# Performance work log

Measured on AMD Instinct MI355X. Metric: run time of the kernel, lower is better.

## Reference

```python
import math
import jax, jax.numpy as jnp
import numpy as np

B, C, L = 4, 768, 8192      # batch, num_channels(width), seq_len
E, O = 33, 64               # emb_dim, order (filter MLP width)


def setup_inputs() -> dict:
    key = jax.random.key(0)
    ks = jax.random.split(key, 8)
    x = jax.random.normal(ks[0], (B, C, L), jnp.float32)
    bias = jax.random.normal(ks[1], (C,), jnp.float32)

    # PositionalEmbedding: z param (constant init) and time_emb t
    t = jnp.linspace(0.0, 1.0, L, dtype=jnp.float32)[None, :, None]   # [1,L,1]
    bands = (E - 1) // 2
    t_r = jnp.linspace(0.0, L - 1.0, L)[None, :, None]
    w = 2.0 * math.pi * t_r / L
    f = jnp.linspace(1e-4, bands - 1.0, bands)[None, None]
    zc = jnp.exp(-1j * f * w)
    z = jnp.concatenate([t, zc.real, zc.imag], axis=2).astype(jnp.float32)  # [1,L,E]

    # ExponentialModulation deltas param (deterministic init)
    target, fast_pct, slow_pct = 0.01, 0.3, 1.5
    max_decay = math.log(target) / fast_pct
    min_decay = math.log(target) / slow_pct
    deltas = jnp.linspace(min_decay, max_decay, C, dtype=jnp.float32)[None, None]  # [1,1,C]

    sc = 0.02
    w0 = jax.random.normal(ks[2], (E, O), jnp.float32) * sc
    b0 = jnp.zeros((O,), jnp.float32)
    w1 = jax.random.normal(ks[3], (O, O), jnp.float32) * sc
    b1 = jnp.zeros((O,), jnp.float32)
    w2 = jax.random.normal(ks[4], (O, O), jnp.float32) * sc
    b2 = jnp.zeros((O,), jnp.float32)
    wout = jax.random.normal(ks[5], (O, C), jnp.float32) * sc  # final Dense, no bias
    freq = jnp.ones((1, O), jnp.float32)  # Sin freq param, shared across all Sin uses
    return dict(x=x, bias=bias, z=z, t=t, deltas=deltas, freq=freq,
                w0=w0, b0=b0, w1=w1, b1=b1, w2=w2, b2=b2, wout=wout)


def reference(x, bias, z, t, deltas, freq, w0, b0, w1, b1, w2, b2, wout):
    seq_len = x.shape[-1]
    # implicit filter MLP: [Dense -> Sin] x3 -> Dense(no bias)
    h = jnp.sin(freq * (z @ w0 + b0))
    h = jnp.sin(freq * (h @ w1 + b1))
    h = jnp.sin(freq * (h @ w2 + b2))
    h = h @ wout                                   # [1, L, C]
    # exponential modulation (shift = 0)
    h = h * jnp.exp(-t * jnp.abs(deltas))          # [1, L, C]
    k = h[0].T                                     # [C, L]
    # FFT long convolution
    fft_size = 2 * seq_len
    k_f = jnp.fft.rfft(k, n=fft_size) / fft_size   # [C, L+1] complex
    u_f = jnp.fft.rfft(x, n=fft_size)              # [B, C, L+1] complex
    y = jnp.fft.irfft(u_f * k_f, n=fft_size, norm='forward')[..., :seq_len]
    out = y + x * bias[:, None]
    return out.astype(x.dtype)
```

## Files before the change

### kernel.cpp

```cpp
#include <hip/hip_runtime.h>
#include <math.h>

#define L_SEQ 8192
#define NFFT  16384
#define N2    8192
#define N4    4096
#define CCH   768
#define BB    4
#define EDIM  33
#define ODIM  64
#define BLK   512

#define C_PI8 0.9238795325112867f
#define S_PI8 0.3826834323650898f
#define C_PI4 0.7071067811865476f

#define ALPHA 1.52587890625e-05f

constexpr int rev4_12c(int v) {
  int r = 0;
  for (int i = 0; i < 6; ++i) { r = (r << 2) | (v & 3); v >>= 2; }
  return r;
}
constexpr int pos8c(int f) { return ((f & 1) << 12) | rev4_12c(f >> 1); }
constexpr int swzc(int i) { return i ^ ((i >> 4) & 15) ^ ((i >> 8) & 15); }

__device__ __forceinline__ float2 cadd(float2 a, float2 b) { return make_float2(a.x + b.x, a.y + b.y); }
__device__ __forceinline__ float2 csub(float2 a, float2 b) { return make_float2(a.x - b.x, a.y - b.y); }
__device__ __forceinline__ float2 cmul(float2 a, float2 b) {
  return make_float2(fmaf(a.x, b.x, -a.y * b.y), fmaf(a.x, b.y, a.y * b.x));
}
__device__ __forceinline__ float2 cmulc(float2 a, float2 w) {
  return make_float2(fmaf(a.x, w.x, a.y * w.y), fmaf(a.y, w.x, -a.x * w.y));
}
__device__ __forceinline__ float2 cconj(float2 a) { return make_float2(a.x, -a.y); }

__device__ __forceinline__ void dif4(float2& x0, float2& x1, float2& x2, float2& x3,
                                     float2 w1, float2 w2, float2 w3) {
  float2 a = cadd(x0, x2), b = csub(x0, x2);
  float2 c = cadd(x1, x3), d = csub(x1, x3);
  x0 = cadd(a, c);
  x1 = cmul(make_float2(b.x + d.y, b.y - d.x), w1);
  x2 = cmul(csub(a, c), w2);
  x3 = cmul(make_float2(b.x - d.y, b.y + d.x), w3);
}
__device__ __forceinline__ void dif4_nw(float2& x0, float2& x1, float2& x2, float2& x3) {
  float2 a = cadd(x0, x2), b = csub(x0, x2);
  float2 c = cadd(x1, x3), d = csub(x1, x3);
  x0 = cadd(a, c);
  x1 = make_float2(b.x + d.y, b.y - d.x);
  x2 = csub(a, c);
  x3 = make_float2(b.x - d.y, b.y + d.x);
}
__device__ __forceinline__ void dit4(float2& x0, float2& x1, float2& x2, float2& x3,
                                     float2 w1, float2 w2, float2 w3) {
  float2 t0 = x0, t1 = cmulc(x1, w1), t2 = cmulc(x2, w2), t3 = cmulc(x3, w3);
  float2 a = cadd(t0, t2), b = csub(t0, t2);
  float2 c = cadd(t1, t3), d = csub(t1, t3);
  x0 = cadd(a, c);
  x1 = make_float2(b.x - d.y, b.y + d.x);
  x2 = csub(a, c);
  x3 = make_float2(b.x + d.y, b.y - d.x);
}
__device__ __forceinline__ void dit4_nw(float2& x0, float2& x1, float2& x2, float2& x3) {
  float2 a = cadd(x0, x2), b = csub(x0, x2);
  float2 c = cadd(x1, x3), d = csub(x1, x3);
  x0 = cadd(a, c);
  x1 = make_float2(b.x - d.y, b.y + d.x);
  x2 = csub(a, c);
  x3 = make_float2(b.x + d.y, b.y - d.x);
}

__device__ __forceinline__ void ld3(const float4* __restrict__ tab, int idx,
                                    float2& w1, float2& w2, float2& w3) {
  float4 a = tab[2 * idx];
  float4 b = tab[2 * idx + 1];
  w1 = make_float2(a.x, a.y);
  w2 = make_float2(a.z, a.w);
  w3 = make_float2(b.x, b.y);
}

__global__ void twiddle_kernel(float2* __restrict__ tw, float4* __restrict__ T4,
                               float4* __restrict__ T16, float4* __restrict__ T64,
                               float4* __restrict__ T256) {
  const int r = blockIdx.x * blockDim.x + threadIdx.x;
  const float C = (float)(6.283185307179586476925286766559 / 16384.0);
  if (r < NFFT) {
    float s, c;
    sincosf(C * (float)r, &s, &c);
    tw[r] = make_float2(c, -s);
  }
  const int j = r - NFFT;
  float4* tab = nullptr;
  int idx = 0, e = 0;
  if (j >= 0 && j < 1024)      { tab = T4;   idx = j;        e = 4 * (j & 255) + 1024 * (j >> 8); }
  else if (j >= 1024 && j < 1280) { tab = T16;  idx = j - 1024; e = 16 * idx; }
  else if (j >= 1280 && j < 1344) { tab = T64;  idx = j - 1280; e = 64 * (idx & 15) + 1024 * (idx >> 4); }
  else if (j >= 1344 && j < 1360) { tab = T256; idx = j - 1344; e = 256 * idx; }
  if (tab) {
    float s1, c1, s2, c2, s3, c3;
    sincosf(C * (float)e, &s1, &c1);
    sincosf(C * (float)(2 * e), &s2, &c2);
    sincosf(C * (float)(3 * e), &s3, &c3);
    tab[2 * idx]     = make_float4(c1, -s1, c2, -s2);
    tab[2 * idx + 1] = make_float4(c3, -s3, 0.f, 0.f);
  }
}

#define ML 16
__global__ __launch_bounds__(128) void mlp_kernel(
    const float* __restrict__ z, const float* __restrict__ freq,
    const float* __restrict__ w0, const float* __restrict__ b0,
    const float* __restrict__ w1, const float* __restrict__ b1,
    const float* __restrict__ w2, const float* __restrict__ b2,
    float* __restrict__ h)
{
  __shared__ float zs[ML][EDIM];
  __shared__ float hsA[ML][ODIM + 1];
  __shared__ float hsB[ML][ODIM + 1];
  const int tid = threadIdx.x;
  const int l0 = blockIdx.x * ML;
  const int lrow = tid & 15;
  const int oc = (tid >> 4) * 8;

  for (int idx = tid; idx < ML * EDIM; idx += 128) {
    int r = idx / EDIM, cc = idx - r * EDIM;
    zs[r][cc] = z[(l0 + r) * EDIM + cc];
  }
  __syncthreads();

  float acc[8], fr[8];
#pragma unroll
  for (int k = 0; k < 8; ++k) { fr[k] = freq[oc + k]; acc[k] = b0[oc + k]; }
#pragma unroll 4
  for (int e = 0; e < EDIM; ++e) {
    const float zv = zs[lrow][e];
#pragma unroll
    for (int j = 0; j < 2; ++j) {
      float4 w4 = *(const float4*)&w0[e * ODIM + oc + 4 * j];
      acc[4*j+0] = fmaf(zv, w4.x, acc[4*j+0]);
      acc[4*j+1] = fmaf(zv, w4.y, acc[4*j+1]);
      acc[4*j+2] = fmaf(zv, w4.z, acc[4*j+2]);
      acc[4*j+3] = fmaf(zv, w4.w, acc[4*j+3]);
    }
  }
#pragma unroll
  for (int k = 0; k < 8; ++k) hsA[lrow][oc + k] = sinf(fr[k] * acc[k]);
  __syncthreads();

#pragma unroll
  for (int k = 0; k < 8; ++k) acc[k] = b1[oc + k];
#pragma unroll 4
  for (int i = 0; i < ODIM; ++i) {
    const float hv = hsA[lrow][i];
#pragma unroll
    for (int j = 0; j < 2; ++j) {
      float4 w4 = *(const float4*)&w1[i * ODIM + oc + 4 * j];
      acc[4*j+0] = fmaf(hv, w4.x, acc[4*j+0]);
      acc[4*j+1] = fmaf(hv, w4.y, acc[4*j+1]);
      acc[4*j+2] = fmaf(hv, w4.z, acc[4*j+2]);
      acc[4*j+3] = fmaf(hv, w4.w, acc[4*j+3]);
    }
  }
#pragma unroll
  for (int k = 0; k < 8; ++k) hsB[lrow][oc + k] = sinf(fr[k] * acc[k]);
  __syncthreads();

#pragma unroll
  for (int k = 0; k < 8; ++k) acc[k] = b2[oc + k];
#pragma unroll 4
  for (int i = 0; i < ODIM; ++i) {
    const float hv = hsB[lrow][i];
#pragma unroll
    for (int j = 0; j < 2; ++j) {
      float4 w4 = *(const float4*)&w2[i * ODIM + oc + 4 * j];
      acc[4*j+0] = fmaf(hv, w4.x, acc[4*j+0]);
      acc[4*j+1] = fmaf(hv, w4.y, acc[4*j+1]);
      acc[4*j+2] = fmaf(hv, w4.z, acc[4*j+2]);
      acc[4*j+3] = fmaf(hv, w4.w, acc[4*j+3]);
    }
  }
#pragma unroll
  for (int k = 0; k < 8; ++k)
    h[(size_t)(oc + k) * L_SEQ + l0 + lrow] = sinf(fr[k] * acc[k]);
}

__global__ __launch_bounds__(256) void kout_kernel(
    const float* __restrict__ h, const float* __restrict__ wout,
    const float* __restrict__ t, const float* __restrict__ deltas,
    float* __restrict__ k)
{
  __shared__ float hT[ODIM][64];
  __shared__ float wT[ODIM][64];
  const int lb = blockIdx.x % (L_SEQ / 64);
  const int cb = blockIdx.x / (L_SEQ / 64);
  const int l0 = lb * 64, c0 = cb * 64;
  const int tid = threadIdx.x;
  for (int i = tid; i < ODIM * 16; i += 256) {
    int o = i >> 4, lq = (i & 15) * 4;
    *(float4*)&hT[o][lq] = *(const float4*)&h[(size_t)o * L_SEQ + l0 + lq];
  }
  for (int i = tid; i < ODIM * 16; i += 256) {
    int o = i >> 4, cq = (i & 15) * 4;
    *(float4*)&wT[o][cq] = *(const float4*)&wout[(size_t)o * CCH + c0 + cq];
  }
  __syncthreads();
  const int li = tid & 15, ci = tid >> 4;
  float acc[4][4];
#pragma unroll
  for (int a = 0; a < 4; ++a)
#pragma unroll
    for (int b = 0; b < 4; ++b) acc[a][b] = 0.f;
#pragma unroll 8
  for (int o = 0; o < ODIM; ++o) {
    float4 h4 = *(const float4*)&hT[o][li * 4];
    float4 w4 = *(const float4*)&wT[o][ci * 4];
    const float ha[4] = {h4.x, h4.y, h4.z, h4.w};
    const float wa[4] = {w4.x, w4.y, w4.z, w4.w};
#pragma unroll
    for (int a = 0; a < 4; ++a)
#pragma unroll
      for (int b = 0; b < 4; ++b) acc[a][b] = fmaf(ha[a], wa[b], acc[a][b]);
  }
  float4 t4 = *(const float4*)&t[l0 + li * 4];
  const float ta[4] = {t4.x, t4.y, t4.z, t4.w};
#pragma unroll
  for (int b = 0; b < 4; ++b) {
    const int c = c0 + ci * 4 + b;
    const float dl = fabsf(deltas[c]);
    float4 r;
    r.x = acc[0][b] * expf(-ta[0] * dl);
    r.y = acc[1][b] * expf(-ta[1] * dl);
    r.z = acc[2][b] * expf(-ta[2] * dl);
    r.w = acc[3][b] * expf(-ta[3] * dl);
    *(float4*)&k[(size_t)c * L_SEQ + l0 + li * 4] = r;
  }
}

__device__ __forceinline__ void load_row(float2 xr[4][4], const float2* __restrict__ src,
                                         const float2* __restrict__ tw, int tid) {
  const int h = tid >> 8, u = tid & 255;
#pragma unroll
  for (int s = 0; s < 4; ++s)
#pragma unroll
    for (int t = 0; t < 4; ++t) xr[s][t] = src[u + s * 1024 + t * 256];
  if (h) {
#pragma unroll
    for (int s = 0; s < 4; ++s)
#pragma unroll
      for (int t = 0; t < 4; ++t) xr[s][t] = cmul(xr[s][t], tw[2 * (u + s * 1024 + t * 256)]);
  }
}

__device__ __forceinline__ void fwd_roundA(float2* Z, float2 xr[4][4],
                                           const float4* __restrict__ T4,
                                           const float4* __restrict__ T16, int tid) {
  const int h = tid >> 8, u = tid & 255;
#pragma unroll
  for (int t = 0; t < 4; ++t) {
    float2 w1, w2, w3;
    ld3(T4, t * 256 + u, w1, w2, w3);
    dif4(xr[0][t], xr[1][t], xr[2][t], xr[3][t], w1, w2, w3);
  }
  {
    float2 w1, w2, w3;
    ld3(T16, u, w1, w2, w3);
#pragma unroll
    for (int s = 0; s < 4; ++s) dif4(xr[s][0], xr[s][1], xr[s][2], xr[s][3], w1, w2, w3);
  }
  const int sb = swzc((h << 12) + u);
#pragma unroll
  for (int s = 0; s < 4; ++s)
#pragma unroll
    for (int t = 0; t < 4; ++t) Z[sb ^ swzc(s * 1024 + t * 256)] = xr[s][t];
}

__device__ __forceinline__ void fwd_roundB(float2* Z, const float4* __restrict__ T64,
                                           const float4* __restrict__ T256, int tid) {
  const int u = tid & 15, g = (tid >> 4) & 15, h = tid >> 8;
  const int sb = swzc((h << 12) + (g << 8) + u);
  float2 e[4][4];
#pragma unroll
  for (int s = 0; s < 4; ++s)
#pragma unroll
    for (int t = 0; t < 4; ++t) e[s][t] = Z[sb ^ swzc(s * 64 + t * 16)];
#pragma unroll
  for (int t = 0; t < 4; ++t) {
    float2 w1, w2, w3;
    ld3(T64, t * 16 + u, w1, w2, w3);
    dif4(e[0][t], e[1][t], e[2][t], e[3][t], w1, w2, w3);
  }
  {
    float2 w1, w2, w3;
    ld3(T256, u, w1, w2, w3);
#pragma unroll
    for (int s = 0; s < 4; ++s) dif4(e[s][0], e[s][1], e[s][2], e[s][3], w1, w2, w3);
  }
#pragma unroll
  for (int s = 0; s < 4; ++s)
#pragma unroll
    for (int t = 0; t < 4; ++t) Z[sb ^ swzc(s * 64 + t * 16)] = e[s][t];
}

__device__ __forceinline__ void fwd_roundC(float2* Z, int tid) {
  const int h = tid >> 8, jp = tid & 255;
  const int sb = swzc((h << 12) + (jp << 4));
  float2 e[4][4];
#pragma unroll
  for (int s = 0; s < 4; ++s)
#pragma unroll
    for (int t = 0; t < 4; ++t) e[s][t] = Z[sb ^ (s * 4 + t)];
  dif4_nw(e[0][0], e[1][0], e[2][0], e[3][0]);
  dif4(e[0][1], e[1][1], e[2][1], e[3][1],
       make_float2(C_PI8, -S_PI8), make_float2(C_PI4, -C_PI4), make_float2(S_PI8, -C_PI8));
  dif4(e[0][2], e[1][2], e[2][2], e[3][2],
       make_float2(C_PI4, -C_PI4), make_float2(0.f, -1.f), make_float2(-C_PI4, -C_PI4));
  dif4(e[0][3], e[1][3], e[2][3], e[3][3],
       make_float2(S_PI8, -C_PI8), make_float2(-C_PI4, -C_PI4), make_float2(-C_PI8, S_PI8));
#pragma unroll
  for (int s = 0; s < 4; ++s) dif4_nw(e[s][0], e[s][1], e[s][2], e[s][3]);
#pragma unroll
  for (int s = 0; s < 4; ++s)
#pragma unroll
    for (int t = 0; t < 4; ++t) Z[sb ^ (s * 4 + t)] = e[s][t];
}

__device__ __forceinline__ void inv_roundA(float2* Z, int tid) {
  const int h = tid >> 8, jp = tid & 255;
  const int sb = swzc((h << 12) + (jp << 4));
  float2 e[4][4];
#pragma unroll
  for (int s = 0; s < 4; ++s)
#pragma unroll
    for (int t = 0; t < 4; ++t) e[s][t] = Z[sb ^ (s * 4 + t)];
#pragma unroll
  for (int s = 0; s < 4; ++s) dit4_nw(e[s][0], e[s][1], e[s][2], e[s][3]);
  dit4_nw(e[0][0], e[1][0], e[2][0], e[3][0]);
  dit4(e[0][1], e[1][1], e[2][1], e[3][1],
       make_float2(C_PI8, -S_PI8), make_float2(C_PI4, -C_PI4), make_float2(S_PI8, -C_PI8));
  dit4(e[0][2], e[1][2], e[2][2], e[3][2],
       make_float2(C_PI4, -C_PI4), make_float2(0.f, -1.f), make_float2(-C_PI4, -C_PI4));
  dit4(e[0][3], e[1][3], e[2][3], e[3][3],
       make_float2(S_PI8, -C_PI8), make_float2(-C_PI4, -C_PI4), make_float2(-C_PI8, S_PI8));
#pragma unroll
  for (int s = 0; s < 4; ++s)
#pragma unroll
    for (int t = 0; t < 4; ++t) Z[sb ^ (s * 4 + t)] = e[s][t];
}

__device__ __forceinline__ void inv_roundB(float2* Z, const float4* __restrict__ T64,
                                           const float4* __restrict__ T256, int tid) {
  const int u = tid & 15, g = (tid >> 4) & 15, h = tid >> 8;
  const int sb = swzc((h << 12) + (g << 8) + u);
  float2 e[4][4];
#pragma unroll
  for (int s = 0; s < 4; ++s)
#pragma unroll
    for (int t = 0; t < 4; ++t) e[s][t] = Z[sb ^ swzc(s * 64 + t * 16)];
  {
    float2 w1, w2, w3;
    ld3(T256, u, w1, w2, w3);
#pragma unroll
    for (int s = 0; s < 4; ++s) dit4(e[s][0], e[s][1], e[s][2], e[s][3], w1, w2, w3);
  }
#pragma unroll
  for (int t = 0; t < 4; ++t) {
    float2 w1, w2, w3;
    ld3(T64, t * 16 + u, w1, w2, w3);
    dit4(e[0][t], e[1][t], e[2][t], e[3][t], w1, w2, w3);
  }
#pragma unroll
  for (int s = 0; s < 4; ++s)
#pragma unroll
    for (int t = 0; t < 4; ++t) Z[sb ^ swzc(s * 64 + t * 16)] = e[s][t];
}

__device__ __forceinline__ void inv_roundC(float2* Z, const float4* __restrict__ T4,
                                           const float4* __restrict__ T16, int tid) {
  const int h = tid >> 8, u = tid & 255;
  const int sb = swzc((h << 12) + u);
  float2 e[4][4];
#pragma unroll
  for (int s = 0; s < 4; ++s)
#pragma unroll
    for (int t = 0; t < 4; ++t) e[s][t] = Z[sb ^ swzc(s * 1024 + t * 256)];
  {
    float2 w1, w2, w3;
    ld3(T16, u, w1, w2, w3);
#pragma unroll
    for (int s = 0; s < 4; ++s) dit4(e[s][0], e[s][1], e[s][2], e[s][3], w1, w2, w3);
  }
#pragma unroll
  for (int t = 0; t < 4; ++t) {
    float2 w1, w2, w3;
    ld3(T4, t * 256 + u, w1, w2, w3);
    dit4(e[0][t], e[1][t], e[2][t], e[3][t], w1, w2, w3);
  }
#pragma unroll
  for (int s = 0; s < 4; ++s)
#pragma unroll
    for (int t = 0; t < 4; ++t) Z[sb ^ swzc(s * 1024 + t * 256)] = e[s][t];
}

__global__ __launch_bounds__(BLK, 4) void kfft_kernel(
    const float* __restrict__ kf, const float2* __restrict__ tw,
    const float4* __restrict__ T4, const float4* __restrict__ T16,
    const float4* __restrict__ T64, const float4* __restrict__ T256,
    float2* __restrict__ Kf)
{
  extern __shared__ float2 Z[];
  const int c = blockIdx.x, tid = threadIdx.x;
  const float2* k2 = (const float2*)(kf + (size_t)c * L_SEQ);
  float2 xr[4][4];
  load_row(xr, k2, tw, tid);
  fwd_roundA(Z, xr, T4, T16, tid);
  __syncthreads();
  fwd_roundB(Z, T64, T256, tid);
  __syncthreads();
  fwd_roundC(Z, tid);
  __syncthreads();

  float2* Kc = Kf + (size_t)c * N2;
  const int P0 = swzc(pos8c(tid));
  const int Q0 = swzc(pos8c(512 - tid));
  const float beta = 0.5f * ALPHA;
#pragma unroll
  for (int s2 = 0; s2 < 8; ++s2) {
    if (s2 == 0 && tid == 0) {
      float2 z0 = Z[0];
      Kc[0] = make_float2(ALPHA * (z0.x + z0.y), ALPHA * (z0.x - z0.y));
      float2 z4 = Z[2];
      Kc[N4] = make_float2(ALPHA * z4.x, -ALPHA * z4.y);
    } else {
      const int f = tid + s2 * BLK;
      const int p = P0 ^ swzc(pos8c(s2 * 512));
      const int pq = (tid == 0) ? swzc(pos8c(((16 - s2) * 512) & (N2 - 1)))
                                : (Q0 ^ swzc(pos8c((15 - s2) * 512)));
      float2 zf = Z[p], zg = Z[pq];
      float2 E = make_float2(beta * (zf.x + zg.x), beta * (zf.y - zg.y));
      float2 O = make_float2(beta * (zf.y + zg.y), beta * (zg.x - zf.x));
      float2 wO = cmul(tw[f], O);
      Kc[f]      = cadd(E, wO);
      Kc[N2 - f] = cconj(csub(E, wO));
    }
  }
}

__global__ __launch_bounds__(BLK, 4) void conv_kernel(
    const float* __restrict__ x, const float2* __restrict__ Kf,
    const float* __restrict__ bias, const float2* __restrict__ tw,
    const float4* __restrict__ T4, const float4* __restrict__ T16,
    const float4* __restrict__ T64, const float4* __restrict__ T256,
    float* __restrict__ out)
{
  extern __shared__ float2 Z[];
  const int tid = threadIdx.x;
  const int c = blockIdx.x % CCH;
  const int b = blockIdx.x / CCH;
  const float2* x2 = (const float2*)(x + (size_t)(b * CCH + c) * L_SEQ);
  const float2* Kc = Kf + (size_t)c * N2;

  float2 xr[4][4];
  load_row(xr, x2, tw, tid);
  fwd_roundA(Z, xr, T4, T16, tid);
  __syncthreads();
  fwd_roundB(Z, T64, T256, tid);
  __syncthreads();
  fwd_roundC(Z, tid);
  __syncthreads();

  const int P0 = swzc(pos8c(tid));
  const int Q0 = swzc(pos8c(512 - tid));
#pragma unroll
  for (int s2 = 0; s2 < 8; ++s2) {
    if (s2 == 0 && tid == 0) {
      float2 z0 = Z[0];
      float2 k0 = Kc[0];
      float2 k4 = Kc[N4];
      float Y0 = (z0.x + z0.y) * k0.x;
      float Y8 = (z0.x - z0.y) * k0.y;
      Z[0] = make_float2(2.f * (Y0 + Y8), 2.f * (Y0 - Y8));
      float2 z4 = Z[2];
      float2 Y4 = cmul(make_float2(z4.x, -z4.y), k4);
      Z[2] = make_float2(4.f * Y4.x, -4.f * Y4.y);
    } else {
      const int f = tid + s2 * BLK;
      const int fc = (N2 - f) & (N2 - 1);
      const int p = P0 ^ swzc(pos8c(s2 * 512));
      const int pq = (tid == 0) ? swzc(pos8c(((16 - s2) * 512) & (N2 - 1)))
                                : (Q0 ^ swzc(pos8c((15 - s2) * 512)));
      float2 k0 = Kc[f];
      float2 k1 = Kc[fc];
      float2 zf = Z[p], zg = Z[pq];
      float2 E = make_float2(zf.x + zg.x, zf.y - zg.y);
      float2 O = make_float2(zf.y + zg.y, zg.x - zf.x);
      float2 w = tw[f];
      float2 wO = cmul(w, O);
      float2 P = cadd(E, wO);
      float2 M = csub(E, wO);
      float2 Yf  = cmul(P, k0);
      float2 Ygc = cmul(M, cconj(k1));
      float2 A  = make_float2(Yf.x + Ygc.x, Yf.y + Ygc.y);
      float2 Bc = make_float2(Yf.x - Ygc.x, Yf.y - Ygc.y);
      float2 cb = cmulc(Bc, w);
      Z[p]  = make_float2(A.x - cb.y, A.y + cb.x);
      Z[pq] = make_float2(A.x + cb.y, -A.y + cb.x);
    }
  }
  __syncthreads();
  inv_roundA(Z, tid);
  __syncthreads();
  inv_roundB(Z, T64, T256, tid);
  __syncthreads();
  inv_roundC(Z, T4, T16, tid);
  __syncthreads();

  const float bc = bias[c];
  float2* o2 = (float2*)(out + (size_t)(b * CCH + c) * L_SEQ);
  const int E0 = swzc(tid);
#pragma unroll
  for (int j = 0; j < 8; ++j) {
    const int i = tid + j * 512;
    const int zi = E0 ^ swzc(j * 512);
    float2 a = Z[zi];
    float2 bb = cmulc(Z[zi ^ 4096], tw[2 * i]);
    float2 xv = x2[i];
    o2[i] = make_float2(a.x + bb.x + xv.x * bc, a.y + bb.y + xv.y * bc);
  }
}

extern "C" void kernel_launch(void* const* d_in, const int* in_sizes, int n_in,
                              void* d_out, int out_size, void* d_ws, size_t ws_size,
                              hipStream_t stream) {
  const float* x      = (const float*)d_in[0];
  const float* bias   = (const float*)d_in[1];
  const float* z      = (const float*)d_in[2];
  const float* t      = (const float*)d_in[3];
  const float* deltas = (const float*)d_in[4];
  const float* freq   = (const float*)d_in[5];
  const float* w0     = (const float*)d_in[6];
  const float* b0     = (const float*)d_in[7];
  const float* w1     = (const float*)d_in[8];
  const float* b1     = (const float*)d_in[9];
  const float* w2     = (const float*)d_in[10];
  const float* b2     = (const float*)d_in[11];
  const float* wout   = (const float*)d_in[12];
  float* out = (float*)d_out;

  char* p = (char*)d_ws;
  float2* tw   = (float2*)p;             p += (size_t)NFFT * sizeof(float2);
  float4* T4   = (float4*)p;             p += (size_t)1024 * 2 * sizeof(float4);
  float4* T16  = (float4*)p;             p += (size_t)256 * 2 * sizeof(float4);
  float4* T64  = (float4*)p;             p += (size_t)64 * 2 * sizeof(float4);
  float4* T256 = (float4*)p;             p += (size_t)16 * 2 * sizeof(float4);
  float*  h    = (float*)p;              p += (size_t)ODIM * L_SEQ * sizeof(float);
  float*  kfilt= (float*)p;              p += (size_t)CCH * L_SEQ * sizeof(float);
  float2* Kf   = (float2*)p;

  twiddle_kernel<<<70, 256, 0, stream>>>(tw, T4, T16, T64, T256);
  mlp_kernel<<<L_SEQ / ML, 128, 0, stream>>>(z, freq, w0, b0, w1, b1, w2, b2, h);
  kout_kernel<<<(L_SEQ / 64) * (CCH / 64), 256, 0, stream>>>(h, wout, t, deltas, kfilt);

  const size_t lds = (size_t)N2 * sizeof(float2);
  hipFuncSetAttribute(reinterpret_cast<const void*>(kfft_kernel),
                      hipFuncAttributeMaxDynamicSharedMemorySize, lds);
  hipFuncSetAttribute(reinterpret_cast<const void*>(conv_kernel),
                      hipFuncAttributeMaxDynamicSharedMemorySize, lds);
  kfft_kernel<<<CCH, BLK, lds, stream>>>(kfilt, tw, T4, T16, T64, T256, Kf);
  conv_kernel<<<BB * CCH, BLK, lds, stream>>>(x, Kf, bias, tw, T4, T16, T64, T256, out);
}
```

Before: 207.3 us.

## Restructure FFT into per-stage radix-4 passes with 1024-thread blocks

Replaces the register-heavy radix-16 rounds, where each thread holds a 4x4 tile, with six radix-4 stages done one at a time in LDS by 1024 threads, each thread processing two butterflies per stage. The first forward stage and the last inverse stage are fused with the global load and the store. The aim is fewer registers per thread and more resident threads to hide memory latency. The cost is twice as many barriers and LDS round trips, plus a 1024-thread block holding 64KB of LDS, which may limit occupancy.

```diff
diff --git a/kernel.cpp b/kernel.cpp
--- a/kernel.cpp
+++ b/kernel.cpp
@@ -9,11 +9,7 @@
 #define BB    4
 #define EDIM  33
 #define ODIM  64
-#define BLK   512
-
-#define C_PI8 0.9238795325112867f
-#define S_PI8 0.3826834323650898f
-#define C_PI4 0.7071067811865476f
+#define BLK2  1024
 
 #define ALPHA 1.52587890625e-05f
 
@@ -237,172 +233,120 @@
   }
 }
 
-__device__ __forceinline__ void load_row(float2 xr[4][4], const float2* __restrict__ src,
-                                         const float2* __restrict__ tw, int tid) {
-  const int h = tid >> 8, u = tid & 255;
-#pragma unroll
-  for (int s = 0; s < 4; ++s)
-#pragma unroll
-    for (int t = 0; t < 4; ++t) xr[s][t] = src[u + s * 1024 + t * 256];
-  if (h) {
-#pragma unroll
-    for (int s = 0; s < 4; ++s)
-#pragma unroll
-      for (int t = 0; t < 4; ++t) xr[s][t] = cmul(xr[s][t], tw[2 * (u + s * 1024 + t * 256)]);
-  }
-}
-
-__device__ __forceinline__ void fwd_roundA(float2* Z, float2 xr[4][4],
-                                           const float4* __restrict__ T4,
-                                           const float4* __restrict__ T16, int tid) {
-  const int h = tid >> 8, u = tid & 255;
-#pragma unroll
-  for (int t = 0; t < 4; ++t) {
-    float2 w1, w2, w3;
-    ld3(T4, t * 256 + u, w1, w2, w3);
-    dif4(xr[0][t], xr[1][t], xr[2][t], xr[3][t], w1, w2, w3);
-  }
-  {
-    float2 w1, w2, w3;
-    ld3(T16, u, w1, w2, w3);
-#pragma unroll
-    for (int s = 0; s < 4; ++s) dif4(xr[s][0], xr[s][1], xr[s][2], xr[s][3], w1, w2, w3);
-  }
-  const int sb = swzc((h << 12) + u);
-#pragma unroll
-  for (int s = 0; s < 4; ++s)
-#pragma unroll
-    for (int t = 0; t < 4; ++t) Z[sb ^ swzc(s * 1024 + t * 256)] = xr[s][t];
-}
-
-__device__ __forceinline__ void fwd_roundB(float2* Z, const float4* __restrict__ T64,
-                                           const float4* __restrict__ T256, int tid) {
-  const int u = tid & 15, g = (tid >> 4) & 15, h = tid >> 8;
-  const int sb = swzc((h << 12) + (g << 8) + u);
-  float2 e[4][4];
-#pragma unroll
-  for (int s = 0; s < 4; ++s)
-#pragma unroll
-    for (int t = 0; t < 4; ++t) e[s][t] = Z[sb ^ swzc(s * 64 + t * 16)];
-#pragma unroll
-  for (int t = 0; t < 4; ++t) {
-    float2 w1, w2, w3;
-    ld3(T64, t * 16 + u, w1, w2, w3);
-    dif4(e[0][t], e[1][t], e[2][t], e[3][t], w1, w2, w3);
-  }
-  {
-    float2 w1, w2, w3;
-    ld3(T256, u, w1, w2, w3);
-#pragma unroll
-    for (int s = 0; s < 4; ++s) dif4(e[s][0], e[s][1], e[s][2], e[s][3], w1, w2, w3);
-  }
-#pragma unroll
-  for (int s = 0; s < 4; ++s)
-#pragma unroll
-    for (int t = 0; t < 4; ++t) Z[sb ^ swzc(s * 64 + t * 16)] = e[s][t];
-}
-
-__device__ __forceinline__ void fwd_roundC(float2* Z, int tid) {
-  const int h = tid >> 8, jp = tid & 255;
-  const int sb = swzc((h << 12) + (jp << 4));
-  float2 e[4][4];
-#pragma unroll
-  for (int s = 0; s < 4; ++s)
-#pragma unroll
-    for (int t = 0; t < 4; ++t) e[s][t] = Z[sb ^ (s * 4 + t)];
-  dif4_nw(e[0][0], e[1][0], e[2][0], e[3][0]);
-  dif4(e[0][1], e[1][1], e[2][1], e[3][1],
-       make_float2(C_PI8, -S_PI8), make_float2(C_PI4, -C_PI4), make_float2(S_PI8, -C_PI8));
-  dif4(e[0][2], e[1][2], e[2][2], e[3][2],
-       make_float2(C_PI4, -C_PI4), make_float2(0.f, -1.f), make_float2(-C_PI4, -C_PI4));
-  dif4(e[0][3], e[1][3], e[2][3], e[3][3],
-       make_float2(S_PI8, -C_PI8), make_float2(-C_PI4, -C_PI4), make_float2(-C_PI8, S_PI8));
-#pragma unroll
-  for (int s = 0; s < 4; ++s) dif4_nw(e[s][0], e[s][1], e[s][2], e[s][3]);
-#pragma unroll
-  for (int s = 0; s < 4; ++s)
-#pragma unroll
-    for (int t = 0; t < 4; ++t) Z[sb ^ (s * 4 + t)] = e[s][t];
-}
-
-__device__ __forceinline__ void inv_roundA(float2* Z, int tid) {
-  const int h = tid >> 8, jp = tid & 255;
-  const int sb = swzc((h << 12) + (jp << 4));
-  float2 e[4][4];
-#pragma unroll
-  for (int s = 0; s < 4; ++s)
-#pragma unroll
-    for (int t = 0; t < 4; ++t) e[s][t] = Z[sb ^ (s * 4 + t)];
-#pragma unroll
-  for (int s = 0; s < 4; ++s) dit4_nw(e[s][0], e[s][1], e[s][2], e[s][3]);
-  dit4_nw(e[0][0], e[1][0], e[2][0], e[3][0]);
-  dit4(e[0][1], e[1][1], e[2][1], e[3][1],
-       make_float2(C_PI8, -S_PI8), make_float2(C_PI4, -C_PI4), make_float2(S_PI8, -C_PI8));
-  dit4(e[0][2], e[1][2], e[2][2], e[3][2],
-       make_float2(C_PI4, -C_PI4), make_float2(0.f, -1.f), make_float2(-C_PI4, -C_PI4));
-  dit4(e[0][3], e[1][3], e[2][3], e[3][3],
-       make_float2(S_PI8, -C_PI8), make_float2(-C_PI4, -C_PI4), make_float2(-C_PI8, S_PI8));
-#pragma unroll
-  for (int s = 0; s < 4; ++s)
-#pragma unroll
-    for (int t = 0; t < 4; ++t) Z[sb ^ (s * 4 + t)] = e[s][t];
-}
-
-__device__ __forceinline__ void inv_roundB(float2* Z, const float4* __restrict__ T64,
-                                           const float4* __restrict__ T256, int tid) {
-  const int u = tid & 15, g = (tid >> 4) & 15, h = tid >> 8;
-  const int sb = swzc((h << 12) + (g << 8) + u);
-  float2 e[4][4];
-#pragma unroll
-  for (int s = 0; s < 4; ++s)
-#pragma unroll
-    for (int t = 0; t < 4; ++t) e[s][t] = Z[sb ^ swzc(s * 64 + t * 16)];
-  {
-    float2 w1, w2, w3;
-    ld3(T256, u, w1, w2, w3);
-#pragma unroll
-    for (int s = 0; s < 4; ++s) dit4(e[s][0], e[s][1], e[s][2], e[s][3], w1, w2, w3);
-  }
-#pragma unroll
-  for (int t = 0; t < 4; ++t) {
-    float2 w1, w2, w3;
-    ld3(T64, t * 16 + u, w1, w2, w3);
-    dit4(e[0][t], e[1][t], e[2][t], e[3][t], w1, w2, w3);
-  }
-#pragma unroll
-  for (int s = 0; s < 4; ++s)
-#pragma unroll
-    for (int t = 0; t < 4; ++t) Z[sb ^ swzc(s * 64 + t * 16)] = e[s][t];
-}
-
-__device__ __forceinline__ void inv_roundC(float2* Z, const float4* __restrict__ T4,
-                                           const float4* __restrict__ T16, int tid) {
-  const int h = tid >> 8, u = tid & 255;
-  const int sb = swzc((h << 12) + u);
-  float2 e[4][4];
-#pragma unroll
-  for (int s = 0; s < 4; ++s)
-#pragma unroll
-    for (int t = 0; t < 4; ++t) e[s][t] = Z[sb ^ swzc(s * 1024 + t * 256)];
-  {
-    float2 w1, w2, w3;
-    ld3(T16, u, w1, w2, w3);
-#pragma unroll
-    for (int s = 0; s < 4; ++s) dit4(e[s][0], e[s][1], e[s][2], e[s][3], w1, w2, w3);
-  }
-#pragma unroll
-  for (int t = 0; t < 4; ++t) {
-    float2 w1, w2, w3;
-    ld3(T4, t * 256 + u, w1, w2, w3);
-    dit4(e[0][t], e[1][t], e[2][t], e[3][t], w1, w2, w3);
-  }
-#pragma unroll
-  for (int s = 0; s < 4; ++s)
-#pragma unroll
-    for (int t = 0; t < 4; ++t) Z[sb ^ swzc(s * 1024 + t * 256)] = e[s][t];
-}
-
-__global__ __launch_bounds__(BLK, 4) void kfft_kernel(
+
+template<int MLOG, int ISCALE>
+__device__ __forceinline__ void stg_fwd(float2* __restrict__ Z,
+                                        const float4* __restrict__ tab, int tid) {
+  constexpr int M = 1 << MLOG;
+  const int u = tid & (M - 1);
+  const int sb = swzc(((tid >> MLOG) << (MLOG + 2)) | u);
+  float2 w1, w2, w3;
+  ld3(tab, u * ISCALE, w1, w2, w3);
+#pragma unroll
+  for (int h = 0; h < 2; ++h) {
+    const int b = sb ^ (h << 12);
+    float2 x0 = Z[b];
+    float2 x1 = Z[b ^ swzc(M)];
+    float2 x2v = Z[b ^ swzc(2 * M)];
+    float2 x3 = Z[b ^ swzc(3 * M)];
+    dif4(x0, x1, x2v, x3, w1, w2, w3);
+    Z[b] = x0;
+    Z[b ^ swzc(M)] = x1;
+    Z[b ^ swzc(2 * M)] = x2v;
+    Z[b ^ swzc(3 * M)] = x3;
+  }
+}
+
+__device__ __forceinline__ void stg_fwd_m1(float2* __restrict__ Z, int tid) {
+  const int sb = swzc(tid << 2);
+#pragma unroll
+  for (int h = 0; h < 2; ++h) {
+    const int b = sb ^ (h << 12);
+    float2 x0 = Z[b], x1 = Z[b ^ 1], x2v = Z[b ^ 2], x3 = Z[b ^ 3];
+    dif4_nw(x0, x1, x2v, x3);
+    Z[b] = x0; Z[b ^ 1] = x1; Z[b ^ 2] = x2v; Z[b ^ 3] = x3;
+  }
+}
+
+template<int MLOG, int ISCALE>
+__device__ __forceinline__ void stg_inv(float2* __restrict__ Z,
+                                        const float4* __restrict__ tab, int tid) {
+  constexpr int M = 1 << MLOG;
+  const int u = tid & (M - 1);
+  const int sb = swzc(((tid >> MLOG) << (MLOG + 2)) | u);
+  float2 w1, w2, w3;
+  ld3(tab, u * ISCALE, w1, w2, w3);
+#pragma unroll
+  for (int h = 0; h < 2; ++h) {
+    const int b = sb ^ (h << 12);
+    float2 x0 = Z[b];
+    float2 x1 = Z[b ^ swzc(M)];
+    float2 x2v = Z[b ^ swzc(2 * M)];
+    float2 x3 = Z[b ^ swzc(3 * M)];
+    dit4(x0, x1, x2v, x3, w1, w2, w3);
+    Z[b] = x0;
+    Z[b ^ swzc(M)] = x1;
+    Z[b ^ swzc(2 * M)] = x2v;
+    Z[b ^ swzc(3 * M)] = x3;
+  }
+}
+
+__device__ __forceinline__ void stg_inv_m1(float2* __restrict__ Z, int tid) {
+  const int sb = swzc(tid << 2);
+#pragma unroll
+  for (int h = 0; h < 2; ++h) {
+    const int b = sb ^ (h << 12);
+    float2 x0 = Z[b], x1 = Z[b ^ 1], x2v = Z[b ^ 2], x3 = Z[b ^ 3];
+    dit4_nw(x0, x1, x2v, x3);
+    Z[b] = x0; Z[b ^ 1] = x1; Z[b ^ 2] = x2v; Z[b ^ 3] = x3;
+  }
+}
+
+__device__ __forceinline__ void fwd_stage1_load(float2* __restrict__ Z,
+                                                const float2* __restrict__ src,
+                                                const float2* __restrict__ tw,
+                                                const float4* __restrict__ T4, int tid) {
+  float2 g[4], o[4];
+#pragma unroll
+  for (int t = 0; t < 4; ++t) g[t] = src[tid + (t << 10)];
+#pragma unroll
+  for (int t = 0; t < 4; ++t) o[t] = cmul(g[t], tw[(tid + (t << 10)) << 1]);
+  float2 w1, w2, w3;
+  ld3(T4, tid, w1, w2, w3);
+  dif4(g[0], g[1], g[2], g[3], w1, w2, w3);
+  dif4(o[0], o[1], o[2], o[3], w1, w2, w3);
+  const int sb = swzc(tid);
+  Z[sb]              = g[0];
+  Z[sb ^ swzc(1024)] = g[1];
+  Z[sb ^ swzc(2048)] = g[2];
+  Z[sb ^ swzc(3072)] = g[3];
+  const int sc = sb ^ 4096;
+  Z[sc]              = o[0];
+  Z[sc ^ swzc(1024)] = o[1];
+  Z[sc ^ swzc(2048)] = o[2];
+  Z[sc ^ swzc(3072)] = o[3];
+}
+
+__device__ __forceinline__ void fft_fwd(float2* __restrict__ Z, const float2* __restrict__ src,
+                                        const float2* __restrict__ tw,
+                                        const float4* __restrict__ T4, const float4* __restrict__ T16,
+                                        const float4* __restrict__ T64, const float4* __restrict__ T256,
+                                        int tid) {
+  fwd_stage1_load(Z, src, tw, T4, tid);
+  __syncthreads();
+  stg_fwd<8, 1>(Z, T16, tid);
+  __syncthreads();
+  stg_fwd<6, 1>(Z, T64, tid);
+  __syncthreads();
+  stg_fwd<4, 1>(Z, T256, tid);
+  __syncthreads();
+  stg_fwd<2, 256>(Z, T4, tid);
+  __syncthreads();
+  stg_fwd_m1(Z, tid);
+  __syncthreads();
+}
+
+__global__ __launch_bounds__(BLK2, 8) void kfft_kernel(
     const float* __restrict__ kf, const float2* __restrict__ tw,
     const float4* __restrict__ T4, const float4* __restrict__ T16,
     const float4* __restrict__ T64, const float4* __restrict__ T256,
@@ -411,31 +355,24 @@
   extern __shared__ float2 Z[];
   const int c = blockIdx.x, tid = threadIdx.x;
   const float2* k2 = (const float2*)(kf + (size_t)c * L_SEQ);
-  float2 xr[4][4];
-  load_row(xr, k2, tw, tid);
-  fwd_roundA(Z, xr, T4, T16, tid);
-  __syncthreads();
-  fwd_roundB(Z, T64, T256, tid);
-  __syncthreads();
-  fwd_roundC(Z, tid);
-  __syncthreads();
+  fft_fwd(Z, k2, tw, T4, T16, T64, T256, tid);
 
   float2* Kc = Kf + (size_t)c * N2;
   const int P0 = swzc(pos8c(tid));
-  const int Q0 = swzc(pos8c(512 - tid));
+  const int Q0 = swzc(pos8c(1024 - tid));
   const float beta = 0.5f * ALPHA;
 #pragma unroll
-  for (int s2 = 0; s2 < 8; ++s2) {
+  for (int s2 = 0; s2 < 4; ++s2) {
     if (s2 == 0 && tid == 0) {
       float2 z0 = Z[0];
       Kc[0] = make_float2(ALPHA * (z0.x + z0.y), ALPHA * (z0.x - z0.y));
       float2 z4 = Z[2];
       Kc[N4] = make_float2(ALPHA * z4.x, -ALPHA * z4.y);
     } else {
-      const int f = tid + s2 * BLK;
-      const int p = P0 ^ swzc(pos8c(s2 * 512));
-      const int pq = (tid == 0) ? swzc(pos8c(((16 - s2) * 512) & (N2 - 1)))
-                                : (Q0 ^ swzc(pos8c((15 - s2) * 512)));
+      const int f = tid + (s2 << 10);
+      const int p = P0 ^ swzc(pos8c(s2 << 10));
+      const int pq = (tid == 0) ? swzc(pos8c((8 - s2) << 10))
+                                : (Q0 ^ swzc(pos8c((7 - s2) << 10)));
       float2 zf = Z[p], zg = Z[pq];
       float2 E = make_float2(beta * (zf.x + zg.x), beta * (zf.y - zg.y));
       float2 O = make_float2(beta * (zf.y + zg.y), beta * (zg.x - zf.x));
@@ -446,7 +383,7 @@
   }
 }
 
-__global__ __launch_bounds__(BLK, 4) void conv_kernel(
+__global__ __launch_bounds__(BLK2, 8) void conv_kernel(
     const float* __restrict__ x, const float2* __restrict__ Kf,
     const float* __restrict__ bias, const float2* __restrict__ tw,
     const float4* __restrict__ T4, const float4* __restrict__ T16,
@@ -460,19 +397,12 @@
   const float2* x2 = (const float2*)(x + (size_t)(b * CCH + c) * L_SEQ);
   const float2* Kc = Kf + (size_t)c * N2;
 
-  float2 xr[4][4];
-  load_row(xr, x2, tw, tid);
-  fwd_roundA(Z, xr, T4, T16, tid);
-  __syncthreads();
-  fwd_roundB(Z, T64, T256, tid);
-  __syncthreads();
-  fwd_roundC(Z, tid);
-  __syncthreads();
+  fft_fwd(Z, x2, tw, T4, T16, T64, T256, tid);
 
   const int P0 = swzc(pos8c(tid));
-  const int Q0 = swzc(pos8c(512 - tid));
-#pragma unroll
-  for (int s2 = 0; s2 < 8; ++s2) {
+  const int Q0 = swzc(pos8c(1024 - tid));
+#pragma unroll
+  for (int s2 = 0; s2 < 4; ++s2) {
     if (s2 == 0 && tid == 0) {
       float2 z0 = Z[0];
       float2 k0 = Kc[0];
@@ -484,13 +414,12 @@
       float2 Y4 = cmul(make_float2(z4.x, -z4.y), k4);
       Z[2] = make_float2(4.f * Y4.x, -4.f * Y4.y);
     } else {
-      const int f = tid + s2 * BLK;
-      const int fc = (N2 - f) & (N2 - 1);
-      const int p = P0 ^ swzc(pos8c(s2 * 512));
-      const int pq = (tid == 0) ? swzc(pos8c(((16 - s2) * 512) & (N2 - 1)))
-                                : (Q0 ^ swzc(pos8c((15 - s2) * 512)));
+      const int f = tid + (s2 << 10);
+      const int p = P0 ^ swzc(pos8c(s2 << 10));
+      const int pq = (tid == 0) ? swzc(pos8c((8 - s2) << 10))
+                                : (Q0 ^ swzc(pos8c((7 - s2) << 10)));
       float2 k0 = Kc[f];
-      float2 k1 = Kc[fc];
+      float2 k1 = Kc[N2 - f];
       float2 zf = Z[p], zg = Z[pq];
       float2 E = make_float2(zf.x + zg.x, zf.y - zg.y);
       float2 O = make_float2(zf.y + zg.y, zg.x - zf.x);
@@ -508,24 +437,40 @@
     }
   }
   __syncthreads();
-  inv_roundA(Z, tid);
-  __syncthreads();
-  inv_roundB(Z, T64, T256, tid);
-  __syncthreads();
-  inv_roundC(Z, T4, T16, tid);
+
+  stg_inv_m1(Z, tid);
+  __syncthreads();
+  stg_inv<2, 256>(Z, T4, tid);
+  __syncthreads();
+  stg_inv<4, 1>(Z, T256, tid);
+  __syncthreads();
+  stg_inv<6, 1>(Z, T64, tid);
+  __syncthreads();
+  stg_inv<8, 1>(Z, T16, tid);
   __syncthreads();
 
   const float bc = bias[c];
   float2* o2 = (float2*)(out + (size_t)(b * CCH + c) * L_SEQ);
-  const int E0 = swzc(tid);
-#pragma unroll
-  for (int j = 0; j < 8; ++j) {
-    const int i = tid + j * 512;
-    const int zi = E0 ^ swzc(j * 512);
-    float2 a = Z[zi];
-    float2 bb = cmulc(Z[zi ^ 4096], tw[2 * i]);
-    float2 xv = x2[i];
-    o2[i] = make_float2(a.x + bb.x + xv.x * bc, a.y + bb.y + xv.y * bc);
+  {
+    float2 w1, w2, w3;
+    ld3(T4, tid, w1, w2, w3);
+    const int sb = swzc(tid);
+    float2 A0 = Z[sb],        A1 = Z[sb ^ swzc(1024)];
+    float2 A2 = Z[sb ^ swzc(2048)], A3 = Z[sb ^ swzc(3072)];
+    dit4(A0, A1, A2, A3, w1, w2, w3);
+    const int sc = sb ^ 4096;
+    float2 B0 = Z[sc],        B1 = Z[sc ^ swzc(1024)];
+    float2 B2 = Z[sc ^ swzc(2048)], B3 = Z[sc ^ swzc(3072)];
+    dit4(B0, B1, B2, B3, w1, w2, w3);
+    float2 Aa[4] = {A0, A1, A2, A3};
+    float2 Bb[4] = {B0, B1, B2, B3};
+#pragma unroll
+    for (int s = 0; s < 4; ++s) {
+      const int i = tid + (s << 10);
+      float2 bb = cmulc(Bb[s], tw[i << 1]);
+      float2 xv = x2[i];
+      o2[i] = make_float2(Aa[s].x + bb.x + xv.x * bc, Aa[s].y + bb.y + xv.y * bc);
+    }
   }
 }
 
@@ -566,6 +511,6 @@
                       hipFuncAttributeMaxDynamicSharedMemorySize, lds);
   hipFuncSetAttribute(reinterpret_cast<const void*>(conv_kernel),
                       hipFuncAttributeMaxDynamicSharedMemorySize, lds);
-  kfft_kernel<<<CCH, BLK, lds, stream>>>(kfilt, tw, T4, T16, T64, T256, Kf);
-  conv_kernel<<<BB * CCH, BLK, lds, stream>>>(x, Kf, bias, tw, T4, T16, T64, T256, out);
-}
+  kfft_kernel<<<CCH, BLK2, lds, stream>>>(kfilt, tw, T4, T16, T64, T256, Kf);
+  conv_kernel<<<BB * CCH, BLK2, lds, stream>>>(x, Kf, bias, tw, T4, T16, T64, T256, out);
+}
```

New measurement: 225.5 us. 8.8% more time.
